# Optimization experiments

Measured on AMD Instinct MI355X. Metric: run time of the kernel, lower is better.

The kernel has to match this reference:

```python
import jax, jax.numpy as jnp
import numpy as np

N_NODES = 50000
N_EDGES = 800000
SD = 128
N_GRAPHS = 128
HL = 4
VOCAB = 1340
N_CLASSES = 41
BN_EPS = 1e-5


def setup_inputs() -> dict:
    key = jax.random.key(0)
    ks = jax.random.split(key, 20)
    s = 1.0 / np.sqrt(SD)
    inp = {
        "node_ids": jax.random.randint(ks[0], (N_NODES,), 0, VOCAB),
        "edge_index": jax.random.randint(ks[1], (2, N_EDGES), 0, N_NODES),
        "batch": jnp.sort(jax.random.randint(ks[2], (N_NODES,), 0, N_GRAPHS)),
        "emb": jax.random.normal(ks[3], (VOCAB, SD)) * 0.05,
        "in_W1": jax.random.normal(ks[4], (SD, SD)) * s,
        "in_b1": jnp.zeros((SD,)),
        "in_W2": jax.random.normal(ks[5], (SD, SD)) * s,
        "in_b2": jnp.zeros((SD,)),
        "bn_gamma": jnp.ones((SD,)),
        "bn_beta": jnp.zeros((SD,)),
        "bn_mean": jnp.zeros((SD,)),
        "bn_var": jnp.ones((SD,)),
        "out_W1": jax.random.normal(ks[6], (SD, SD)) * s,
        "out_b1": jnp.zeros((SD,)),
        "out_W2": jax.random.normal(ks[7], (SD, SD)) * s,
        "out_b2": jnp.zeros((SD,)),
        "fc1_W": jax.random.normal(ks[8], (SD, SD)) * s,
        "fc1_b": jnp.zeros((SD,)),
        "fc2_W": jax.random.normal(ks[9], (N_CLASSES, SD)) * s,
        "fc2_b": jnp.zeros((N_CLASSES,)),
    }
    return inp


def reference(node_ids, edge_index, batch, emb, in_W1, in_b1, in_W2, in_b2,
              bn_gamma, bn_beta, bn_mean, bn_var,
              out_W1, out_b1, out_W2, out_b2, fc1_W, fc1_b, fc2_W, fc2_b):
    src, dst = edge_index[0], edge_index[1]

    def gin(x, W1, b1, W2, b2):
        # GINConv with eps=0: mlp(x + sum_{j in N(i)} x_j)
        agg = jax.ops.segment_sum(x[src], dst, num_segments=N_NODES)
        h = x + agg
        h = jnp.maximum(h @ W1.T + b1, 0.0)
        return h @ W2.T + b2

    def bn(x):
        # eval-mode BatchNorm1d with running stats
        return (x - bn_mean) * (bn_gamma / jnp.sqrt(bn_var + BN_EPS)) + bn_beta

    x = emb[node_ids]  # [N, SD]
    x = bn(jnp.maximum(gin(x, in_W1, in_b1, in_W2, in_b2), 0.0))
    for _ in range(HL):  # shared weights, repeated hl times
        x = bn(jnp.maximum(gin(x, in_W1, in_b1, in_W2, in_b2), 0.0))
    x = jnp.maximum(gin(x, out_W1, out_b1, out_W2, out_b2), 0.0)
    pooled = jax.ops.segment_sum(x, batch, num_segments=N_GRAPHS)  # [G, SD]
    h = jnp.maximum(pooled @ fc1_W.T + fc1_b, 0.0)
    return h @ fc2_W.T + fc2_b  # [G, 41]
```

## Files before the change

### kernel.cpp

```cpp
#include <hip/hip_runtime.h>

#define NN 50000
#define NE 800000
#define NG 128
#define NC 41
#define CAP 64
#define XG 8
#define RNG 6250

typedef __attribute__((ext_vector_type(8))) short bfrag8;
typedef __attribute__((ext_vector_type(4))) float facc4;

__device__ __forceinline__ float bf2f(unsigned short u) {
  union { unsigned int i; float f; } v; v.i = ((unsigned int)u) << 16; return v.f;
}
__device__ __forceinline__ unsigned short f2bf(float f) {
  union { float f; unsigned int i; } v; v.f = f;
  unsigned int x = v.i;
  x += 0x7fffu + ((x >> 16) & 1u);
  return (unsigned short)(x >> 16);
}
__device__ __forceinline__ void acc_u4(const uint4 u, float* a) {
  union { unsigned int i; float f; } c;
  c.i = u.x << 16;          a[0] += c.f;
  c.i = u.x & 0xffff0000u;  a[1] += c.f;
  c.i = u.y << 16;          a[2] += c.f;
  c.i = u.y & 0xffff0000u;  a[3] += c.f;
  c.i = u.z << 16;          a[4] += c.f;
  c.i = u.z & 0xffff0000u;  a[5] += c.f;
  c.i = u.w << 16;          a[6] += c.f;
  c.i = u.w & 0xffff0000u;  a[7] += c.f;
}
__device__ __forceinline__ unsigned int pack2(float lo, float hi) {
  return (unsigned int)f2bf(lo) | ((unsigned int)f2bf(hi) << 16);
}

__global__ void prep_kernel(const float* __restrict__ W1, const float* __restrict__ W2,
                            const float* __restrict__ oW1, const float* __restrict__ oW2,
                            const float* __restrict__ gamma, const float* __restrict__ beta,
                            const float* __restrict__ mean, const float* __restrict__ var,
                            unsigned short* W1b, unsigned short* W2b,
                            unsigned short* oW1b, unsigned short* oW2b,
                            float* scale, float* shift) {
  int i = blockIdx.x * 256 + threadIdx.x;
  if (i < 128 * 128) {
    W1b[i] = f2bf(W1[i]);
    W2b[i] = f2bf(W2[i]);
    oW1b[i] = f2bf(oW1[i]);
    oW2b[i] = f2bf(oW2[i]);
  }
  if (i < 128) {
    float s = gamma[i] * rsqrtf(var[i] + 1e-5f);
    scale[i] = s;
    shift[i] = beta[i] - mean[i] * s;
  }
}

__global__ void embed_kernel(const int* __restrict__ node_ids, const float* __restrict__ emb,
                             unsigned short* __restrict__ xb) {
  int idx = blockIdx.x * 256 + threadIdx.x;
  if (idx >= NN * 32) return;
  int node = idx >> 5, f = (idx & 31) * 4;
  const float4 v = *(const float4*)&emb[node_ids[node] * 128 + f];
  ushort4 o;
  o.x = f2bf(v.x); o.y = f2bf(v.y); o.z = f2bf(v.z); o.w = f2bf(v.w);
  *(ushort4*)&xb[node * 128 + f] = o;
}

__global__ __launch_bounds__(256) void fill_kernel(const int* __restrict__ ei,
                                                   int* __restrict__ cnt,
                                                   unsigned short* __restrict__ srclist) {
  int b = blockIdx.x;
  int g = b & 7;
  int s = b >> 3;
  int e = s * 256 + threadIdx.x;
  if (e >= NE) return;
  int d = ei[NE + e];
  unsigned int lo = g * RNG;
  if ((unsigned int)(d - lo) < (unsigned int)RNG) {
    int src = ei[e];
    int pos = atomicAdd(&cnt[d], 1);
    if (pos < CAP) srclist[d * CAP + pos] = (unsigned short)src;
  }
}

__global__ __launch_bounds__(256) void gin_layer_kernel(
    const unsigned short* __restrict__ xin,
    const int* __restrict__ cnt,
    const unsigned short* __restrict__ srclist,
    const unsigned short* __restrict__ W1b,
    const unsigned short* __restrict__ W2b,
    const float* __restrict__ bias1,
    const float* __restrict__ bias2,
    const float* __restrict__ scale,
    const float* __restrict__ shift,
    unsigned short* __restrict__ Out,
    const int* __restrict__ batch,
    float* __restrict__ pooled,
    int M, int mode, int doPool) {
  __shared__ unsigned short sW[128 * 128];
  __shared__ unsigned short sA[64 * 128];
  int tid = threadIdx.x;
  int bRow = blockIdx.x * 64;

  const uint4* gw1 = (const uint4*)W1b;
#pragma unroll
  for (int p = 0; p < 8; ++p) {
    int g = p * 256 + tid;
    int r = g >> 4, b = g & 15;
    int ph = (b + r) & 15;
    *(uint4*)&sW[(r * 16 + ph) * 8] = gw1[g];
  }

  {
    int al16 = tid & 15;
    int sub = tid >> 4;
    int f = al16 * 8;

    int n0 = bRow + sub, n1 = n0 + 16, n2 = n0 + 32, n3 = n0 + 48;
    int d0 = (n0 < M) ? cnt[n0] : 0;
    int d1 = (n1 < M) ? cnt[n1] : 0;
    int d2 = (n2 < M) ? cnt[n2] : 0;
    int d3 = (n3 < M) ? cnt[n3] : 0;

#pragma unroll 1
    for (int g = 0; g < 4; ++g) {
      int r = g * 16 + sub;
      int node = bRow + r;
      float a[8];
      a[0]=0.f; a[1]=0.f; a[2]=0.f; a[3]=0.f;
      a[4]=0.f; a[5]=0.f; a[6]=0.f; a[7]=0.f;
      if (node < M) {
        int deg = (g == 0) ? d0 : (g == 1) ? d1 : (g == 2) ? d2 : d3;
        if (deg > CAP) deg = CAP;
        const unsigned short* lst = &srclist[node * CAP];
        acc_u4(*(const uint4*)&xin[node * 128 + f], a);
        int j = 0;
#pragma unroll 1
        for (; j + 16 <= deg; j += 16) {
          uint4 iv0 = *(const uint4*)&lst[j];
          uint4 iv1 = *(const uint4*)&lst[j + 8];
          int p0 = iv0.x & 0xffff, p1 = iv0.x >> 16;
          int p2 = iv0.y & 0xffff, p3 = iv0.y >> 16;
          int p4 = iv0.z & 0xffff, p5 = iv0.z >> 16;
          int p6 = iv0.w & 0xffff, p7 = iv0.w >> 16;
          uint4 uA0 = *(const uint4*)&xin[p0 * 128 + f];
          uint4 uA1 = *(const uint4*)&xin[p1 * 128 + f];
          uint4 uA2 = *(const uint4*)&xin[p2 * 128 + f];
          uint4 uA3 = *(const uint4*)&xin[p3 * 128 + f];
          uint4 uA4 = *(const uint4*)&xin[p4 * 128 + f];
          uint4 uA5 = *(const uint4*)&xin[p5 * 128 + f];
          uint4 uA6 = *(const uint4*)&xin[p6 * 128 + f];
          uint4 uA7 = *(const uint4*)&xin[p7 * 128 + f];
          int q0 = iv1.x & 0xffff, q1 = iv1.x >> 16;
          int q2 = iv1.y & 0xffff, q3 = iv1.y >> 16;
          int q4 = iv1.z & 0xffff, q5 = iv1.z >> 16;
          int q6 = iv1.w & 0xffff, q7 = iv1.w >> 16;
          uint4 uB0 = *(const uint4*)&xin[q0 * 128 + f];
          uint4 uB1 = *(const uint4*)&xin[q1 * 128 + f];
          uint4 uB2 = *(const uint4*)&xin[q2 * 128 + f];
          uint4 uB3 = *(const uint4*)&xin[q3 * 128 + f];
          uint4 uB4 = *(const uint4*)&xin[q4 * 128 + f];
          uint4 uB5 = *(const uint4*)&xin[q5 * 128 + f];
          uint4 uB6 = *(const uint4*)&xin[q6 * 128 + f];
          uint4 uB7 = *(const uint4*)&xin[q7 * 128 + f];
          acc_u4(uA0, a); acc_u4(uA1, a); acc_u4(uA2, a); acc_u4(uA3, a);
          acc_u4(uA4, a); acc_u4(uA5, a); acc_u4(uA6, a); acc_u4(uA7, a);
          acc_u4(uB0, a); acc_u4(uB1, a); acc_u4(uB2, a); acc_u4(uB3, a);
          acc_u4(uB4, a); acc_u4(uB5, a); acc_u4(uB6, a); acc_u4(uB7, a);
        }
        if (j + 8 <= deg) {
          uint4 iv = *(const uint4*)&lst[j];
          int p0 = iv.x & 0xffff, p1 = iv.x >> 16;
          int p2 = iv.y & 0xffff, p3 = iv.y >> 16;
          int p4 = iv.z & 0xffff, p5 = iv.z >> 16;
          int p6 = iv.w & 0xffff, p7 = iv.w >> 16;
          uint4 u0 = *(const uint4*)&xin[p0 * 128 + f];
          uint4 u1 = *(const uint4*)&xin[p1 * 128 + f];
          uint4 u2 = *(const uint4*)&xin[p2 * 128 + f];
          uint4 u3 = *(const uint4*)&xin[p3 * 128 + f];
          uint4 u4 = *(const uint4*)&xin[p4 * 128 + f];
          uint4 u5 = *(const uint4*)&xin[p5 * 128 + f];
          uint4 u6 = *(const uint4*)&xin[p6 * 128 + f];
          uint4 u7 = *(const uint4*)&xin[p7 * 128 + f];
          acc_u4(u0, a); acc_u4(u1, a); acc_u4(u2, a); acc_u4(u3, a);
          acc_u4(u4, a); acc_u4(u5, a); acc_u4(u6, a); acc_u4(u7, a);
          j += 8;
        }
        if (j + 4 <= deg) {
          uint2 iv = *(const uint2*)&lst[j];
          int p0 = iv.x & 0xffff, p1 = iv.x >> 16;
          int p2 = iv.y & 0xffff, p3 = iv.y >> 16;
          uint4 u0 = *(const uint4*)&xin[p0 * 128 + f];
          uint4 u1 = *(const uint4*)&xin[p1 * 128 + f];
          uint4 u2 = *(const uint4*)&xin[p2 * 128 + f];
          uint4 u3 = *(const uint4*)&xin[p3 * 128 + f];
          acc_u4(u0, a); acc_u4(u1, a); acc_u4(u2, a); acc_u4(u3, a);
          j += 4;
        }
        for (; j < deg; ++j) {
          uint4 u = *(const uint4*)&xin[(int)lst[j] * 128 + f];
          acc_u4(u, a);
        }
      }
      int ph = (al16 + r) & 15;
      uint4 o;
      o.x = pack2(a[0], a[1]); o.y = pack2(a[2], a[3]);
      o.z = pack2(a[4], a[5]); o.w = pack2(a[6], a[7]);
      *(uint4*)&sA[(r * 16 + ph) * 8] = o;
    }
  }
  __syncthreads();

  int wave = tid >> 6;
  int lane = tid & 63;
  int l16 = lane & 15;
  int quad = lane >> 4;
  int arow = wave * 16 + l16;

  {
    bfrag8 af[4];
#pragma unroll
    for (int k = 0; k < 4; ++k) {
      int ph = (k * 4 + quad + arow) & 15;
      af[k] = *(const bfrag8*)&sA[(arow * 16 + ph) * 8];
    }
    facc4 acc[8];
#pragma unroll
    for (int t = 0; t < 8; ++t) acc[t] = (facc4){0.f, 0.f, 0.f, 0.f};
#pragma unroll
    for (int k = 0; k < 4; ++k) {
#pragma unroll
      for (int t = 0; t < 8; ++t) {
        int r = t * 16 + l16;
        int ph = (k * 4 + quad + r) & 15;
        bfrag8 bf = *(const bfrag8*)&sW[(r * 16 + ph) * 8];
        acc[t] = __builtin_amdgcn_mfma_f32_16x16x32_bf16(af[k], bf, acc[t], 0, 0, 0);
      }
    }
#pragma unroll
    for (int t = 0; t < 8; ++t) {
      int col = t * 16 + l16;
      float b = bias1[col];
      int cb = col >> 3, ce = col & 7;
#pragma unroll
      for (int i = 0; i < 4; ++i) {
        int row = wave * 16 + quad * 4 + i;
        float v = acc[t][i] + b;
        int ph = (cb + row) & 15;
        sA[(row * 16 + ph) * 8 + ce] = f2bf(v > 0.f ? v : 0.f);
      }
    }
  }
  __syncthreads();

  const uint4* gw2 = (const uint4*)W2b;
#pragma unroll
  for (int p = 0; p < 8; ++p) {
    int g = p * 256 + tid;
    int r = g >> 4, b = g & 15;
    int ph = (b + r) & 15;
    *(uint4*)&sW[(r * 16 + ph) * 8] = gw2[g];
  }
  __syncthreads();

  {
    bfrag8 af[4];
#pragma unroll
    for (int k = 0; k < 4; ++k) {
      int ph = (k * 4 + quad + arow) & 15;
      af[k] = *(const bfrag8*)&sA[(arow * 16 + ph) * 8];
    }
    facc4 acc[8];
#pragma unroll
    for (int t = 0; t < 8; ++t) acc[t] = (facc4){0.f, 0.f, 0.f, 0.f};
#pragma unroll
    for (int k = 0; k < 4; ++k) {
#pragma unroll
      for (int t = 0; t < 8; ++t) {
        int r = t * 16 + l16;
        int ph = (k * 4 + quad + r) & 15;
        bfrag8 bf = *(const bfrag8*)&sW[(r * 16 + ph) * 8];
        acc[t] = __builtin_amdgcn_mfma_f32_16x16x32_bf16(af[k], bf, acc[t], 0, 0, 0);
      }
    }
#pragma unroll
    for (int t = 0; t < 8; ++t) {
      int col = t * 16 + l16;
      float b = bias2[col];
      float sc = 1.f, sh = 0.f;
      if (mode == 1) { sc = scale[col]; sh = shift[col]; }
      int cb = col >> 3, ce = col & 7;
#pragma unroll
      for (int i = 0; i < 4; ++i) {
        int row = wave * 16 + quad * 4 + i;
        float v = acc[t][i] + b;
        v = v > 0.f ? v : 0.f;
        if (mode == 1) v = v * sc + sh;
        int ph = (cb + row) & 15;
        sA[(row * 16 + ph) * 8 + ce] = f2bf(v);
      }
    }
  }
  __syncthreads();

  if (doPool) {
    if (tid < 128) {
      int fcol = tid;
      int cb = fcol >> 3, ce = fcol & 7;
      float acc = 0.f;
      int cur = -1;
      for (int r = 0; r < 64; ++r) {
        int row = bRow + r;
        if (row >= M) break;
        int b = batch[row];
        if (b != cur) {
          if (cur >= 0) atomicAdd(&pooled[cur * 128 + fcol], acc);
          cur = b;
          acc = 0.f;
        }
        int ph = (cb + r) & 15;
        acc += bf2f(sA[(r * 16 + ph) * 8 + ce]);
      }
      if (cur >= 0) atomicAdd(&pooled[cur * 128 + fcol], acc);
    }
  } else {
#pragma unroll
    for (int p = 0; p < 4; ++p) {
      int g = p * 256 + tid;
      int r = g >> 4, b = g & 15;
      int ph = (b + r) & 15;
      int grow = bRow + r;
      if (grow < M)
        *(uint4*)&Out[grow * 128 + b * 8] = *(const uint4*)&sA[(r * 16 + ph) * 8];
    }
  }
}

__global__ __launch_bounds__(128) void fc_kernel(const float* __restrict__ pooled,
                                                 const float* __restrict__ W1,
                                                 const float* __restrict__ b1,
                                                 const float* __restrict__ W2,
                                                 const float* __restrict__ b2,
                                                 float* __restrict__ out) {
  __shared__ float sh1[128];
  __shared__ float sp[128];
  int r = blockIdx.x;
  int c = threadIdx.x;
  sp[c] = pooled[r * 128 + c];
  __syncthreads();
  float acc = 0.f;
  for (int k = 0; k < 128; ++k) acc += sp[k] * W1[c * 128 + k];
  acc += b1[c];
  sh1[c] = acc > 0.f ? acc : 0.f;
  __syncthreads();
  if (c < NC) {
    float o = 0.f;
    for (int k = 0; k < 128; ++k) o += sh1[k] * W2[c * 128 + k];
    out[r * NC + c] = o + b2[c];
  }
}

extern "C" void kernel_launch(void* const* d_in, const int* in_sizes, int n_in,
                              void* d_out, int out_size, void* d_ws, size_t ws_size,
                              hipStream_t stream) {
  const int* node_ids = (const int*)d_in[0];
  const int* edge_index = (const int*)d_in[1];
  const int* batch = (const int*)d_in[2];
  const float* emb = (const float*)d_in[3];
  const float* in_W1 = (const float*)d_in[4];
  const float* in_b1 = (const float*)d_in[5];
  const float* in_W2 = (const float*)d_in[6];
  const float* in_b2 = (const float*)d_in[7];
  const float* bn_gamma = (const float*)d_in[8];
  const float* bn_beta = (const float*)d_in[9];
  const float* bn_mean = (const float*)d_in[10];
  const float* bn_var = (const float*)d_in[11];
  const float* out_W1 = (const float*)d_in[12];
  const float* out_b1 = (const float*)d_in[13];
  const float* out_W2 = (const float*)d_in[14];
  const float* out_b2 = (const float*)d_in[15];
  const float* fc1_W = (const float*)d_in[16];
  const float* fc1_b = (const float*)d_in[17];
  const float* fc2_W = (const float*)d_in[18];
  const float* fc2_b = (const float*)d_in[19];
  float* out = (float*)d_out;

  char* ws = (char*)d_ws;
  size_t off = 0;
  auto alloc = [&](size_t bytes) {
    char* p = ws + off;
    off = (off + bytes + 255) & ~(size_t)255;
    return p;
  };
  unsigned short* xb = (unsigned short*)alloc((size_t)NN * 128 * 2);
  unsigned short* hb = (unsigned short*)alloc((size_t)NN * 128 * 2);
  unsigned short* srclist = (unsigned short*)alloc((size_t)NN * CAP * 2);
  int* cnt = (int*)alloc((size_t)NN * 4);
  unsigned short* W1b = (unsigned short*)alloc(128 * 128 * 2);
  unsigned short* W2b = (unsigned short*)alloc(128 * 128 * 2);
  unsigned short* oW1b = (unsigned short*)alloc(128 * 128 * 2);
  unsigned short* oW2b = (unsigned short*)alloc(128 * 128 * 2);
  float* bnscale = (float*)alloc(128 * 4);
  float* bnshift = (float*)alloc(128 * 4);
  float* pooled = (float*)alloc(NG * 128 * 4);

  hipMemsetAsync(cnt, 0, (size_t)NN * 4, stream);
  hipMemsetAsync(pooled, 0, (size_t)NG * 128 * 4, stream);

  prep_kernel<<<64, 256, 0, stream>>>(in_W1, in_W2, out_W1, out_W2,
                                      bn_gamma, bn_beta, bn_mean, bn_var,
                                      W1b, W2b, oW1b, oW2b, bnscale, bnshift);
  int chunks = (NE + 255) / 256;
  fill_kernel<<<chunks * XG, 256, 0, stream>>>(edge_index, cnt, srclist);
  embed_kernel<<<(NN * 32 + 255) / 256, 256, 0, stream>>>(node_ids, emb, xb);

  int mlp_blocks = (NN + 63) / 64;
  const unsigned short* cur = xb;
  unsigned short* nxt = hb;
  for (int l = 0; l < 6; ++l) {
    const unsigned short* w1 = (l < 5) ? W1b : oW1b;
    const unsigned short* w2 = (l < 5) ? W2b : oW2b;
    const float* b1 = (l < 5) ? in_b1 : out_b1;
    const float* b2 = (l < 5) ? in_b2 : out_b2;
    int mode2 = (l < 5) ? 1 : 0;
    int doPool = (l == 5) ? 1 : 0;
    gin_layer_kernel<<<mlp_blocks, 256, 0, stream>>>(
        cur, cnt, srclist, w1, w2, b1, b2, bnscale, bnshift,
        nxt, batch, pooled, NN, mode2, doPool);
    const unsigned short* t = cur;
    cur = nxt;
    nxt = (unsigned short*)t;
  }

  fc_kernel<<<NG, 128, 0, stream>>>(pooled, fc1_W, fc1_b, fc2_W, fc2_b, out);
}
```

Before: 485.4 us.

## Preload both weight matrices and make each wave own its rows to drop barriers

Loads W1 and W2 into separate shared buffers up front and remaps the aggregation, pooling and store phases so each wave handles only its own 16 rows. This removes the block-wide barriers between aggregation, the two MFMA stages and the epilogue, leaving a single sync after the weight load, so waves can run through the pipeline independently. The cost is more LDS per block (two 32KB weight tiles plus the activation tile). A launch-bounds hint of two blocks per CU is added to go with that larger footprint. Pooling now issues per-wave partial atomics, which means more atomic traffic.

```diff
diff --git a/kernel.cpp b/kernel.cpp
--- a/kernel.cpp
+++ b/kernel.cpp
@@ -84,7 +84,7 @@
   }
 }
 
-__global__ __launch_bounds__(256) void gin_layer_kernel(
+__global__ __launch_bounds__(256, 2) void gin_layer_kernel(
     const unsigned short* __restrict__ xin,
     const int* __restrict__ cnt,
     const unsigned short* __restrict__ srclist,
@@ -98,26 +98,33 @@
     const int* __restrict__ batch,
     float* __restrict__ pooled,
     int M, int mode, int doPool) {
-  __shared__ unsigned short sW[128 * 128];
+  __shared__ unsigned short sW1[128 * 128];
+  __shared__ unsigned short sW2[128 * 128];
   __shared__ unsigned short sA[64 * 128];
   int tid = threadIdx.x;
   int bRow = blockIdx.x * 64;
+  int wave = tid >> 6;
+  int lane = tid & 63;
 
   const uint4* gw1 = (const uint4*)W1b;
+  const uint4* gw2 = (const uint4*)W2b;
 #pragma unroll
   for (int p = 0; p < 8; ++p) {
     int g = p * 256 + tid;
     int r = g >> 4, b = g & 15;
     int ph = (b + r) & 15;
-    *(uint4*)&sW[(r * 16 + ph) * 8] = gw1[g];
-  }
+    *(uint4*)&sW1[(r * 16 + ph) * 8] = gw1[g];
+    *(uint4*)&sW2[(r * 16 + ph) * 8] = gw2[g];
+  }
+  __syncthreads();
 
   {
-    int al16 = tid & 15;
-    int sub = tid >> 4;
+    int al16 = lane & 15;
+    int sub4 = lane >> 4;
     int f = al16 * 8;
 
-    int n0 = bRow + sub, n1 = n0 + 16, n2 = n0 + 32, n3 = n0 + 48;
+    int n0 = bRow + wave * 16 + sub4;
+    int n1 = n0 + 4, n2 = n0 + 8, n3 = n0 + 12;
     int d0 = (n0 < M) ? cnt[n0] : 0;
     int d1 = (n1 < M) ? cnt[n1] : 0;
     int d2 = (n2 < M) ? cnt[n2] : 0;
@@ -125,7 +132,7 @@
 
 #pragma unroll 1
     for (int g = 0; g < 4; ++g) {
-      int r = g * 16 + sub;
+      int r = wave * 16 + g * 4 + sub4;
       int node = bRow + r;
       float a[8];
       a[0]=0.f; a[1]=0.f; a[2]=0.f; a[3]=0.f;
@@ -210,10 +217,7 @@
       *(uint4*)&sA[(r * 16 + ph) * 8] = o;
     }
   }
-  __syncthreads();
-
-  int wave = tid >> 6;
-  int lane = tid & 63;
+
   int l16 = lane & 15;
   int quad = lane >> 4;
   int arow = wave * 16 + l16;
@@ -234,7 +238,7 @@
       for (int t = 0; t < 8; ++t) {
         int r = t * 16 + l16;
         int ph = (k * 4 + quad + r) & 15;
-        bfrag8 bf = *(const bfrag8*)&sW[(r * 16 + ph) * 8];
+        bfrag8 bf = *(const bfrag8*)&sW1[(r * 16 + ph) * 8];
         acc[t] = __builtin_amdgcn_mfma_f32_16x16x32_bf16(af[k], bf, acc[t], 0, 0, 0);
       }
     }
@@ -252,17 +256,6 @@
       }
     }
   }
-  __syncthreads();
-
-  const uint4* gw2 = (const uint4*)W2b;
-#pragma unroll
-  for (int p = 0; p < 8; ++p) {
-    int g = p * 256 + tid;
-    int r = g >> 4, b = g & 15;
-    int ph = (b + r) & 15;
-    *(uint4*)&sW[(r * 16 + ph) * 8] = gw2[g];
-  }
-  __syncthreads();
 
   {
     bfrag8 af[4];
@@ -280,7 +273,7 @@
       for (int t = 0; t < 8; ++t) {
         int r = t * 16 + l16;
         int ph = (k * 4 + quad + r) & 15;
-        bfrag8 bf = *(const bfrag8*)&sW[(r * 16 + ph) * 8];
+        bfrag8 bf = *(const bfrag8*)&sW2[(r * 16 + ph) * 8];
         acc[t] = __builtin_amdgcn_mfma_f32_16x16x32_bf16(af[k], bf, acc[t], 0, 0, 0);
       }
     }
@@ -302,15 +295,16 @@
       }
     }
   }
-  __syncthreads();
 
   if (doPool) {
-    if (tid < 128) {
-      int fcol = tid;
+#pragma unroll
+    for (int cc = 0; cc < 2; ++cc) {
+      int fcol = lane + cc * 64;
       int cb = fcol >> 3, ce = fcol & 7;
       float acc = 0.f;
       int cur = -1;
-      for (int r = 0; r < 64; ++r) {
+      for (int s = 0; s < 16; ++s) {
+        int r = wave * 16 + s;
         int row = bRow + r;
         if (row >= M) break;
         int b = batch[row];
@@ -327,8 +321,8 @@
   } else {
 #pragma unroll
     for (int p = 0; p < 4; ++p) {
-      int g = p * 256 + tid;
-      int r = g >> 4, b = g & 15;
+      int r = wave * 16 + p * 4 + (lane >> 4);
+      int b = lane & 15;
       int ph = (b + r) & 15;
       int grow = bRow + r;
       if (grow < M)
```

Result: no change. 488.5 us (+0.6%).
